# Optimization experiments

Hardware: AMD Instinct MI355X
Metric: run time of the kernel (lower is better)

The kernel has to match this reference:

```python
import jax, jax.numpy as jnp
import numpy as np
from jax import lax

EPS = 1e-5
HEADS = 8

def chan_ln(x, g):
    # ChanLayerNorm: normalize over channel dim (1), biased variance, gamma only
    mean = jnp.mean(x, axis=1, keepdims=True)
    var = jnp.var(x, axis=1, keepdims=True)
    return (x - mean) * lax.rsqrt(var + EPS) * g[None, :, None, None]

def conv1x1(x, w):  # w: [O, C]
    return jnp.einsum('bchw,oc->bohw', x, w)

def dwconv3(x, w):  # depthwise 3x3, w: [C,1,3,3]
    return lax.conv_general_dilated(x, w, (1, 1), 'SAME',
                                    dimension_numbers=('NCHW', 'OIHW', 'NCHW'),
                                    feature_group_count=x.shape[1])


def setup_inputs() -> dict:
    key = jax.random.key(0)
    ks = jax.random.split(key, 8)
    B, DIM, H, W = 8, 512, 96, 96
    INNER = 256
    s = 0.02
    return {
        'fmap': jax.random.normal(ks[0], (B, DIM, H, W), jnp.float32),
        'norm_g': jnp.ones((DIM,), jnp.float32),
        'q_w1': jax.random.normal(ks[1], (INNER, DIM), jnp.float32) * s,
        'q_wd': jax.random.normal(ks[2], (INNER, 1, 3, 3), jnp.float32) * s,
        'k_w1': jax.random.normal(ks[3], (INNER, DIM), jnp.float32) * s,
        'k_wd': jax.random.normal(ks[4], (INNER, 1, 3, 3), jnp.float32) * s,
        'v_w1': jax.random.normal(ks[5], (INNER, DIM), jnp.float32) * s,
        'v_wd': jax.random.normal(ks[6], (INNER, 1, 3, 3), jnp.float32) * s,
        'out_w': jax.random.normal(ks[7], (DIM, INNER), jnp.float32) * s,
        'out_norm_g': jnp.ones((DIM,), jnp.float32),
    }


def reference(fmap, norm_g, q_w1, q_wd, k_w1, k_wd, v_w1, v_wd, out_w, out_norm_g):
    B, C, H, W = fmap.shape
    inner = q_w1.shape[0]
    dh = inner // HEADS
    scale = dh ** -0.5

    x = chan_ln(fmap, norm_g)
    # dropout is identity in eval mode
    q = dwconv3(conv1x1(x, q_w1), q_wd)
    k = dwconv3(conv1x1(x, k_w1), k_wd)
    v = dwconv3(conv1x1(x, v_w1), v_wd)

    def split(t):  # [B, h*c, H, W] -> [B*h, N, c]
        return t.reshape(B, HEADS, dh, H * W).transpose(0, 1, 3, 2).reshape(B * HEADS, H * W, dh)

    q, k, v = split(q), split(k), split(v)
    q = jax.nn.softmax(q, axis=-1) * scale   # softmax over feature dim
    k = jax.nn.softmax(k, axis=-2)           # softmax over spatial dim

    context = jnp.einsum('bnd,bne->bde', k, v)   # [B*h, d, d]
    out = jnp.einsum('bnd,bde->bne', q, context) # [B*h, N, d]

    out = out.reshape(B, HEADS, H * W, dh).transpose(0, 1, 3, 2).reshape(B, inner, H, W)
    out = jax.nn.silu(out)
    out = conv1x1(out, out_w)
    return chan_ln(out, out_norm_g)
```

## Files before the change

### kernel.cpp

```cpp
#include <hip/hip_runtime.h>
#include <math.h>

#define BATCH 8
#define GB 4
#define CDIM 512
#define HGT 96
#define WID 96
#define HWN (HGT*WID)
#define INNER 256
#define NHEADS 8
#define DH 32
#define NPIX (BATCH*HWN)
#define EPSLN 1e-5f
#define QSCALE 0.17677669529663687f
#define PATHSZ ((size_t)GB*INNER*HWN)

typedef __bf16 bf16_t;
typedef bf16_t bf16x8 __attribute__((ext_vector_type(8)));
typedef float  f32x4  __attribute__((ext_vector_type(4)));

__device__ __forceinline__ void load_lds16(const bf16_t* gp, bf16_t* lp) {
    __builtin_amdgcn_global_load_lds(
        (const __attribute__((address_space(1))) unsigned int*)gp,
        (__attribute__((address_space(3))) unsigned int*)lp,
        16, 0, 0);
}

__global__ __launch_bounds__(256) void wsum_kernel(const float* __restrict__ qw,
                                                   const float* __restrict__ kw,
                                                   const float* __restrict__ vw,
                                                   const float* __restrict__ g,
                                                   float* __restrict__ wsum) {
    int i = blockIdx.x * 256 + threadIdx.x;
    if (i >= 3 * INNER) return;
    const float* w = (i < INNER) ? qw : (i < 2 * INNER) ? kw : vw;
    int o = i % INNER;
    float s = 0.f;
    for (int c = 0; c < CDIM; ++c) s += w[o * CDIM + c] * g[c];
    wsum[i] = s;
}

__global__ __launch_bounds__(256) void wprep_kernel(const float* __restrict__ qw,
                                                    const float* __restrict__ kw,
                                                    const float* __restrict__ vw,
                                                    const float* __restrict__ g,
                                                    const float* __restrict__ ow,
                                                    bf16_t* __restrict__ WB,
                                                    bf16_t* __restrict__ OWB) {
    int i = blockIdx.x * 256 + threadIdx.x;
    const int PS = INNER * CDIM;
    if (i < 3 * PS) {
        int m = i / PS;
        int idx = i % PS;
        int c = idx % CDIM;
        const float* w = (m == 0) ? qw : (m == 1) ? kw : vw;
        float val = w[idx] * g[c];
        bf16_t h = (bf16_t)val;
        bf16_t l = (bf16_t)(val - (float)h);
        WB[(size_t)(2 * m) * PS + idx] = h;
        WB[(size_t)(2 * m + 1) * PS + idx] = l;
    } else {
        int idx = i - 3 * PS;
        float val = ow[idx];
        bf16_t h = (bf16_t)val;
        bf16_t l = (bf16_t)(val - (float)h);
        OWB[idx] = h;
        OWB[PS + idx] = l;
    }
}

__global__ __launch_bounds__(256) void transpose_split_kernel(const float* __restrict__ X,
                                                              bf16_t* __restrict__ Fh,
                                                              bf16_t* __restrict__ Fl,
                                                              float* __restrict__ S1,
                                                              float* __restrict__ S2,
                                                              int pbase) {
    __shared__ float T[64][65];
    __shared__ float Ps[4][64], Ps2[4][64];
    int bb = blockIdx.z;
    int n0 = blockIdx.x * 64;
    int c0 = blockIdx.y * 64;
    const float* Xb = X + ((size_t)bb * CDIM) * HWN;
    int tid = threadIdx.x;
    int tx = tid & 63, ty = tid >> 6;
    #pragma unroll
    for (int cc = 0; cc < 64; cc += 4)
        T[cc + ty][tx] = Xb[(size_t)(c0 + cc + ty) * HWN + n0 + tx];
    __syncthreads();
    {
        float s = 0.f, s2 = 0.f;
        #pragma unroll
        for (int c = ty * 16; c < ty * 16 + 16; ++c) {
            float v = T[c][tx];
            s += v; s2 += v * v;
        }
        Ps[ty][tx] = s; Ps2[ty][tx] = s2;
    }
    __syncthreads();
    if (tid < 64) {
        float a = Ps[0][tid] + Ps[1][tid] + Ps[2][tid] + Ps[3][tid];
        float b = Ps2[0][tid] + Ps2[1][tid] + Ps2[2][tid] + Ps2[3][tid];
        int p = pbase + bb * HWN + n0 + tid;
        atomicAdd(&S1[p], a);
        atomicAdd(&S2[p], b);
    }
    int nr = tid >> 3;
    int c8 = (tid & 7) << 3;
    size_t obase = ((size_t)bb * HWN) * CDIM;
    #pragma unroll
    for (int half = 0; half < 2; ++half) {
        int n = nr + 32 * half;
        bf16x8 hv, lv;
        #pragma unroll
        for (int j = 0; j < 8; ++j) {
            float v = T[c8 + j][n];
            bf16_t h = (bf16_t)v;
            hv[j] = h;
            lv[j] = (bf16_t)(v - (float)h);
        }
        size_t off = obase + (size_t)(n0 + n) * CDIM + c0 + c8;
        *(bf16x8*)&Fh[off] = hv;
        *(bf16x8*)&Fl[off] = lv;
    }
}

template <int KDIM, int MROWS, int MODE>
__global__ __launch_bounds__(256) void mfma_gemm_kernel(const bf16_t* __restrict__ Wbase,
                                                        const bf16_t* __restrict__ Bh,
                                                        const bf16_t* __restrict__ Bl,
                                                        float* __restrict__ S1,
                                                        float* __restrict__ S2,
                                                        const float* __restrict__ wsum,
                                                        int pbase,
                                                        float* __restrict__ Ybase) {
    __shared__ bf16_t sA[2][128 * 32];
    __shared__ bf16_t sB[2][128 * 32];
    int bb = blockIdx.z;
    int n0 = blockIdx.x * 128;
    const int PS = INNER * CDIM;
    int o0, path;
    const bf16_t *Ah, *Al;
    float* Y;
    if (MODE == 0) {
        path = blockIdx.y >> 1;
        o0 = (blockIdx.y & 1) * 128;
        Ah = Wbase + (size_t)(2 * path) * PS;
        Al = Wbase + (size_t)(2 * path + 1) * PS;
        Y = Ybase + (size_t)path * PATHSZ;
        wsum += path * INNER;
    } else {
        path = 0;
        o0 = blockIdx.y * 128;
        Ah = Wbase;
        Al = Wbase + PS;
        Y = Ybase;
    }
    int tid = threadIdx.x;
    int wv = tid >> 6, ln = tid & 63;
    int wm = wv >> 1, wn = wv & 1;
    int quad = ln >> 4, lm = ln & 15;
    int srow = ln >> 2;
    int scol = (ln & 3) * 8;

    const bf16_t* Bhb = Bh + ((size_t)bb * HWN) * KDIM;
    const bf16_t* Blb = Bl + ((size_t)bb * HWN) * KDIM;

    f32x4 acc[4][4] = {};

    for (int c0 = 0; c0 < KDIM; c0 += 32) {
        __syncthreads();
        #pragma unroll
        for (int t = 0; t < 2; ++t) {
            int inst = wv * 2 + t;
            int row = inst * 16 + srow;
            size_t goA = (size_t)(o0 + row) * KDIM + c0 + scol;
            size_t goB = (size_t)(n0 + row) * KDIM + c0 + scol;
            load_lds16(&Ah[goA],  &sA[0][inst * 512]);
            load_lds16(&Al[goA],  &sA[1][inst * 512]);
            load_lds16(&Bhb[goB], &sB[0][inst * 512]);
            load_lds16(&Blb[goB], &sB[1][inst * 512]);
        }
        __syncthreads();

        bf16x8 afh[4], afl[4], bfh[4], bfl[4];
        #pragma unroll
        for (int i = 0; i < 4; ++i) {
            int o_l = wm * 64 + i * 16 + lm;
            afh[i] = *(const bf16x8*)&sA[0][o_l * 32 + quad * 8];
            afl[i] = *(const bf16x8*)&sA[1][o_l * 32 + quad * 8];
            int n_l = wn * 64 + i * 16 + lm;
            bfh[i] = *(const bf16x8*)&sB[0][n_l * 32 + quad * 8];
            bfl[i] = *(const bf16x8*)&sB[1][n_l * 32 + quad * 8];
        }
        #pragma unroll
        for (int i = 0; i < 4; ++i)
            #pragma unroll
            for (int j = 0; j < 4; ++j) {
                acc[i][j] = __builtin_amdgcn_mfma_f32_16x16x32_bf16(afh[i], bfh[j], acc[i][j], 0, 0, 0);
                acc[i][j] = __builtin_amdgcn_mfma_f32_16x16x32_bf16(afh[i], bfl[j], acc[i][j], 0, 0, 0);
                acc[i][j] = __builtin_amdgcn_mfma_f32_16x16x32_bf16(afl[i], bfh[j], acc[i][j], 0, 0, 0);
            }
    }

    float* Yb = Y + ((size_t)bb * MROWS) * HWN;
    __shared__ float Sn[128], Sn2[128];
    if (MODE == 1) {
        if (tid < 128) Sn[tid] = 0.f; else Sn2[tid - 128] = 0.f;
        __syncthreads();
    }
    #pragma unroll
    for (int j = 0; j < 4; ++j) {
        int nl = wn * 64 + j * 16 + lm;
        int n = n0 + nl;
        float mn = 0.f, rs = 0.f;
        if (MODE == 0) {
            int p = pbase + bb * HWN + n;
            float s1 = S1[p], s2 = S2[p];
            mn = s1 * (1.0f / CDIM);
            float var = s2 * (1.0f / CDIM) - mn * mn;
            rs = rsqrtf(var + EPSLN);
        }
        float js = 0.f, js2 = 0.f;
        #pragma unroll
        for (int i = 0; i < 4; ++i) {
            #pragma unroll
            for (int r = 0; r < 4; ++r) {
                int o = o0 + wm * 64 + i * 16 + quad * 4 + r;
                float v = acc[i][j][r];
                if (MODE == 0) v = rs * (v - mn * wsum[o]);
                Yb[(size_t)o * HWN + n] = v;
                if (MODE == 1) { js += v; js2 += v * v; }
            }
        }
        if (MODE == 1) {
            atomicAdd(&Sn[nl], js);
            atomicAdd(&Sn2[nl], js2);
        }
    }
    if (MODE == 1) {
        __syncthreads();
        if (tid < 128) {
            int p = pbase + bb * HWN + n0 + tid;
            atomicAdd(&S1[p], Sn[tid]);
            atomicAdd(&S2[p], Sn2[tid]);
        }
    }
}

__global__ __launch_bounds__(256) void dwconv_kernel(const float* __restrict__ A3,
                                                     const float* __restrict__ qwd,
                                                     const float* __restrict__ kwd,
                                                     const float* __restrict__ vwd,
                                                     float* __restrict__ D3,
                                                     float* __restrict__ Ssum,
                                                     int bo) {
    int c = blockIdx.y;
    int zz = blockIdx.z;
    int path = zz >> 2;
    int bb = zz & 3;
    const float* wf = ((path == 0) ? qwd : (path == 1) ? kwd : vwd) + c * 9;
    float w[9];
    #pragma unroll
    for (int j = 0; j < 9; ++j) w[j] = wf[j];

    int n0 = (blockIdx.x << 10) + (threadIdx.x << 2);
    int y = n0 / WID;
    int x0 = n0 - y * WID;
    bool hasL = (x0 != 0);
    bool hasR = (x0 != WID - 4);

    const float* bp = A3 + (size_t)path * PATHSZ + (size_t)(bb * INNER + c) * HWN;
    float o0 = 0.f, o1 = 0.f, o2 = 0.f, o3 = 0.f;
    #pragma unroll
    for (int dy = 0; dy < 3; ++dy) {
        int yy = y + dy - 1;
        if ((unsigned)yy < HGT) {
            const float* r = bp + yy * WID + x0;
            f32x4 cv = *(const f32x4*)r;
            float lft = hasL ? r[-1] : 0.f;
            float rgt = hasR ? r[4]  : 0.f;
            float w0 = w[3 * dy], w1 = w[3 * dy + 1], w2 = w[3 * dy + 2];
            o0 += lft  * w0 + cv.x * w1 + cv.y * w2;
            o1 += cv.x * w0 + cv.y * w1 + cv.z * w2;
            o2 += cv.y * w0 + cv.z * w1 + cv.w * w2;
            o3 += cv.z * w0 + cv.w * w1 + rgt  * w2;
        }
    }

    size_t oi = (size_t)path * PATHSZ + (size_t)(bb * INNER + c) * HWN + n0;
    if (path == 1) {
        float e0 = __expf(o0), e1 = __expf(o1), e2 = __expf(o2), e3 = __expf(o3);
        *(f32x4*)&D3[oi] = (f32x4){e0, e1, e2, e3};
        float s = e0 + e1 + e2 + e3;
        #pragma unroll
        for (int off2 = 32; off2; off2 >>= 1) s += __shfl_down(s, off2);
        __shared__ float red[4];
        int lane = threadIdx.x & 63, wvi = threadIdx.x >> 6;
        if (lane == 0) red[wvi] = s;
        __syncthreads();
        if (threadIdx.x == 0)
            atomicAdd(&Ssum[(bo + bb) * INNER + c], red[0] + red[1] + red[2] + red[3]);
    } else {
        *(f32x4*)&D3[oi] = (f32x4){o0, o1, o2, o3};
    }
}

__global__ __launch_bounds__(256) void context_kernel(const float* __restrict__ K,
                                                      const float* __restrict__ V,
                                                      float* __restrict__ ctxp) {
    int seg = blockIdx.x;
    int bh = blockIdx.y;
    int bb = bh / NHEADS, h = bh % NHEADS;
    const float* kb = K + ((size_t)bb * INNER + h * DH) * HWN;
    const float* vb = V + ((size_t)bb * INNER + h * DH) * HWN;
    __shared__ float kt[DH][64];
    __shared__ float vt[DH][65];
    int tid = threadIdx.x;
    int e = tid & 31;
    int d0 = tid >> 5;
    float acc[4] = {0.f, 0.f, 0.f, 0.f};
    for (int ch = 0; ch < 9; ++ch) {
        int n0 = seg * 576 + ch * 64;
        __syncthreads();
        #pragma unroll
        for (int j = 0; j < 8; ++j) {
            int idx = tid + 256 * j;
            int d = idx >> 6, nn = idx & 63;
            kt[d][nn] = kb[(size_t)d * HWN + n0 + nn];
            vt[d][nn] = vb[(size_t)d * HWN + n0 + nn];
        }
        __syncthreads();
        for (int nn = 0; nn < 64; ++nn) {
            float vv = vt[e][nn];
            #pragma unroll
            for (int i = 0; i < 4; ++i) acc[i] += kt[d0 + 8 * i][nn] * vv;
        }
    }
    #pragma unroll
    for (int i = 0; i < 4; ++i)
        ctxp[(((size_t)bh * 16 + seg) * DH + d0 + 8 * i) * DH + e] = acc[i];
}

__global__ __launch_bounds__(256) void ctxreduce_kernel(const float* __restrict__ ctxp,
                                                        const float* __restrict__ Ssum,
                                                        int bo,
                                                        float* __restrict__ ctx) {
    int i = blockIdx.x * 256 + threadIdx.x;
    int bh = i >> 10, de = i & 1023;
    int d = de >> 5;
    int bb = bh / NHEADS, h = bh % NHEADS;
    float s = 0.f;
    #pragma unroll
    for (int seg = 0; seg < 16; ++seg) s += ctxp[((size_t)bh * 16 + seg) * 1024 + de];
    float S = Ssum[(bo + bb) * INNER + h * DH + d];
    ctx[i] = s / S;
}

__global__ __launch_bounds__(256) void qctx_kernel(const float* __restrict__ Q,
                                                   const float* __restrict__ ctx,
                                                   bf16_t* __restrict__ Oh,
                                                   bf16_t* __restrict__ Ol) {
    int bh = blockIdx.y;
    int bb = bh / NHEADS, h = bh % NHEADS;
    int n = blockIdx.x * 256 + threadIdx.x;
    __shared__ float cs[DH * DH];
    for (int j = threadIdx.x; j < DH * DH; j += 256) cs[j] = ctx[(size_t)bh * DH * DH + j];
    __syncthreads();
    const float* qb = Q + ((size_t)bb * INNER + h * DH) * HWN + n;
    float qv[DH];
    float mx = -1e30f;
    #pragma unroll
    for (int d = 0; d < DH; ++d) { qv[d] = qb[(size_t)d * HWN]; mx = fmaxf(mx, qv[d]); }
    float s = 0.f;
    #pragma unroll
    for (int d = 0; d < DH; ++d) { qv[d] = __expf(qv[d] - mx); s += qv[d]; }
    float inv = QSCALE / s;
    float acc[DH];
    #pragma unroll
    for (int e = 0; e < DH; ++e) acc[e] = 0.f;
    #pragma unroll
    for (int d = 0; d < DH; ++d) {
        float q = qv[d] * inv;
        #pragma unroll
        for (int e = 0; e < DH; ++e) acc[e] += q * cs[d * DH + e];
    }
    size_t ob = ((size_t)bb * HWN + n) * INNER + h * DH;
    bf16x8 hv, lv;
    #pragma unroll
    for (int e8 = 0; e8 < 4; ++e8) {
        #pragma unroll
        for (int e = 0; e < 8; ++e) {
            float x = acc[e8 * 8 + e];
            float sl = x / (1.0f + __expf(-x));
            bf16_t h = (bf16_t)sl;
            hv[e] = h;
            lv[e] = (bf16_t)(sl - (float)h);
        }
        *(bf16x8*)&Oh[ob + e8 * 8] = hv;
        *(bf16x8*)&Ol[ob + e8 * 8] = lv;
    }
}

__global__ __launch_bounds__(256) void norm_kernel(const float* __restrict__ X,
                                                   const float* __restrict__ S1,
                                                   const float* __restrict__ S2,
                                                   const float* __restrict__ g,
                                                   float* __restrict__ out,
                                                   int pbase) {
    size_t i = ((size_t)blockIdx.x * 256 + threadIdx.x) * 4;
    int n = (int)(i % HWN);
    size_t bc = i / HWN;
    int c = (int)(bc % CDIM);
    int bb = (int)(bc / CDIM);
    int p = pbase + bb * HWN + n;
    f32x4 x  = *(const f32x4*)&X[i];
    f32x4 s1 = *(const f32x4*)&S1[p];
    f32x4 s2 = *(const f32x4*)&S2[p];
    float gc = g[c];
    f32x4 o;
    #pragma unroll
    for (int j = 0; j < 4; ++j) {
        float m = s1[j] * (1.0f / CDIM);
        float var = s2[j] * (1.0f / CDIM) - m * m;
        float rs = rsqrtf(var + EPSLN);
        o[j] = (x[j] - m) * rs * gc;
    }
    *(f32x4*)&out[i] = o;
}

extern "C" void kernel_launch(void* const* d_in, const int* in_sizes, int n_in,
                              void* d_out, int out_size, void* d_ws, size_t ws_size,
                              hipStream_t stream) {
    const float* fmap       = (const float*)d_in[0];
    const float* norm_g     = (const float*)d_in[1];
    const float* q_w1       = (const float*)d_in[2];
    const float* q_wd       = (const float*)d_in[3];
    const float* k_w1       = (const float*)d_in[4];
    const float* k_wd       = (const float*)d_in[5];
    const float* v_w1       = (const float*)d_in[6];
    const float* v_wd       = (const float*)d_in[7];
    const float* out_w      = (const float*)d_in[8];
    const float* out_norm_g = (const float*)d_in[9];
    float* out = (float*)d_out;

    float* ws = (float*)d_ws;
    size_t off = 0;
    auto alloc = [&](size_t n) { float* p = ws + off; off += n; return p; };
    float* S1   = alloc(73728);
    float* S2   = alloc(73728);
    float* S1o  = alloc(73728);
    float* S2o  = alloc(73728);
    float* Ssum = alloc(2048);
    const size_t ZERON = 73728ull * 4 + 2048;
    float* wsum = alloc(768);
    bf16_t* WB  = (bf16_t*)alloc(393216);
    bf16_t* OWB = (bf16_t*)alloc(131072);
    float* ctxp = alloc(524288);
    float* ctx  = alloc(32768);
    bf16_t* Fh  = (bf16_t*)alloc(9437184);
    bf16_t* Fl  = (bf16_t*)alloc(9437184);
    float* A3   = alloc(3 * 9437184);
    float* D3   = alloc(3 * 9437184);
    bf16_t* Oh  = (bf16_t*)alloc(4718592);
    bf16_t* Ol  = (bf16_t*)alloc(4718592);
    float* CONV2 = alloc(18874368);

    dim3 blk(256);
    hipMemsetAsync(S1, 0, ZERON * sizeof(float), stream);
    wsum_kernel<<<dim3(3), blk, 0, stream>>>(q_w1, k_w1, v_w1, norm_g, wsum);
    wprep_kernel<<<dim3(2048), blk, 0, stream>>>(q_w1, k_w1, v_w1, norm_g, out_w, WB, OWB);

    for (int g = 0; g < 2; ++g) {
        const float* fmg = fmap + (size_t)g * GB * CDIM * HWN;
        int pbase = g * GB * HWN;
        int bo = g * GB;

        transpose_split_kernel<<<dim3(144, 8, GB), blk, 0, stream>>>(fmg, Fh, Fl, S1, S2, pbase);

        mfma_gemm_kernel<CDIM, INNER, 0><<<dim3(72, 6, GB), blk, 0, stream>>>(
            WB, Fh, Fl, S1, S2, wsum, pbase, A3);

        dwconv_kernel<<<dim3(HWN / 1024, INNER, 3 * GB), blk, 0, stream>>>(
            A3, q_wd, k_wd, v_wd, D3, Ssum, bo);

        context_kernel<<<dim3(16, GB * NHEADS), blk, 0, stream>>>(
            D3 + PATHSZ, D3 + 2 * PATHSZ, ctxp);
        ctxreduce_kernel<<<dim3(GB * NHEADS * 1024 / 256), blk, 0, stream>>>(
            ctxp, Ssum, bo, ctx);
        qctx_kernel<<<dim3(HWN / 256, GB * NHEADS), blk, 0, stream>>>(D3, ctx, Oh, Ol);

        mfma_gemm_kernel<INNER, CDIM, 1><<<dim3(72, 4, GB), blk, 0, stream>>>(
            OWB, Oh, Ol, S1o, S2o, nullptr, pbase, CONV2);

        norm_kernel<<<dim3(GB * CDIM * HWN / 1024), blk, 0, stream>>>(
            CONV2, S1o, S2o, out_norm_g, out + (size_t)g * GB * CDIM * HWN, pbase);
    }
}
```

Baseline: 871.2 us.

## Vectorize transpose loads, swizzle GEMM LDS, and compute two rows per dwconv thread

The transpose kernel now reads the input with 16-byte vector loads instead of scalar loads. The MFMA GEMM applies an XOR swizzle to the LDS column offsets on both the global-to-LDS store and the fragment reads, to cut LDS bank conflicts. The depthwise conv is relaunched with 24x8 thread blocks, and each thread computes two output rows from four loaded input rows, so the overlapping row loads are shared. The tradeoffs are more registers per dwconv thread, a smaller block that gives a different reduction layout for the K softmax sum, and a swizzle that must match exactly between the write and read sides.

```diff
diff --git a/kernel.cpp b/kernel.cpp
--- a/kernel.cpp
+++ b/kernel.cpp
@@ -82,10 +82,20 @@
     int c0 = blockIdx.y * 64;
     const float* Xb = X + ((size_t)bb * CDIM) * HWN;
     int tid = threadIdx.x;
+    {
+        int nl4 = (tid & 15) * 4;
+        int cl = tid >> 4;
+        #pragma unroll
+        for (int it = 0; it < 4; ++it) {
+            int cc = cl + 16 * it;
+            f32x4 v = *(const f32x4*)&Xb[(size_t)(c0 + cc) * HWN + n0 + nl4];
+            T[cc][nl4]     = v.x;
+            T[cc][nl4 + 1] = v.y;
+            T[cc][nl4 + 2] = v.z;
+            T[cc][nl4 + 3] = v.w;
+        }
+    }
     int tx = tid & 63, ty = tid >> 6;
-    #pragma unroll
-    for (int cc = 0; cc < 64; cc += 4)
-        T[cc + ty][tx] = Xb[(size_t)(c0 + cc + ty) * HWN + n0 + tx];
     __syncthreads();
     {
         float s = 0.f, s2 = 0.f;
@@ -160,7 +170,8 @@
     int wm = wv >> 1, wn = wv & 1;
     int quad = ln >> 4, lm = ln & 15;
     int srow = ln >> 2;
-    int scol = (ln & 3) * 8;
+    int scol = ((ln & 3) ^ ((ln >> 3) & 3)) * 8;
+    int qs = (quad ^ ((lm >> 1) & 3)) * 8;
 
     const bf16_t* Bhb = Bh + ((size_t)bb * HWN) * KDIM;
     const bf16_t* Blb = Bl + ((size_t)bb * HWN) * KDIM;
@@ -186,11 +197,11 @@
         #pragma unroll
         for (int i = 0; i < 4; ++i) {
             int o_l = wm * 64 + i * 16 + lm;
-            afh[i] = *(const bf16x8*)&sA[0][o_l * 32 + quad * 8];
-            afl[i] = *(const bf16x8*)&sA[1][o_l * 32 + quad * 8];
+            afh[i] = *(const bf16x8*)&sA[0][o_l * 32 + qs];
+            afl[i] = *(const bf16x8*)&sA[1][o_l * 32 + qs];
             int n_l = wn * 64 + i * 16 + lm;
-            bfh[i] = *(const bf16x8*)&sB[0][n_l * 32 + quad * 8];
-            bfl[i] = *(const bf16x8*)&sB[1][n_l * 32 + quad * 8];
+            bfh[i] = *(const bf16x8*)&sB[0][n_l * 32 + qs];
+            bfl[i] = *(const bf16x8*)&sB[1][n_l * 32 + qs];
         }
         #pragma unroll
         for (int i = 0; i < 4; ++i)
@@ -247,7 +258,7 @@
     }
 }
 
-__global__ __launch_bounds__(256) void dwconv_kernel(const float* __restrict__ A3,
+__global__ __launch_bounds__(192) void dwconv_kernel(const float* __restrict__ A3,
                                                      const float* __restrict__ qwd,
                                                      const float* __restrict__ kwd,
                                                      const float* __restrict__ vwd,
@@ -263,45 +274,70 @@
     #pragma unroll
     for (int j = 0; j < 9; ++j) w[j] = wf[j];
 
-    int n0 = (blockIdx.x << 10) + (threadIdx.x << 2);
-    int y = n0 / WID;
-    int x0 = n0 - y * WID;
+    int x0 = threadIdx.x * 4;
+    int y0 = (blockIdx.x * 8 + threadIdx.y) * 2;
     bool hasL = (x0 != 0);
     bool hasR = (x0 != WID - 4);
 
     const float* bp = A3 + (size_t)path * PATHSZ + (size_t)(bb * INNER + c) * HWN;
-    float o0 = 0.f, o1 = 0.f, o2 = 0.f, o3 = 0.f;
-    #pragma unroll
-    for (int dy = 0; dy < 3; ++dy) {
-        int yy = y + dy - 1;
+    f32x4 r[4];
+    float L[4], R[4];
+    #pragma unroll
+    for (int dy = 0; dy < 4; ++dy) {
+        int yy = y0 + dy - 1;
         if ((unsigned)yy < HGT) {
-            const float* r = bp + yy * WID + x0;
-            f32x4 cv = *(const f32x4*)r;
-            float lft = hasL ? r[-1] : 0.f;
-            float rgt = hasR ? r[4]  : 0.f;
+            const float* rp = bp + yy * WID + x0;
+            r[dy] = *(const f32x4*)rp;
+            L[dy] = hasL ? rp[-1] : 0.f;
+            R[dy] = hasR ? rp[4]  : 0.f;
+        } else {
+            r[dy] = (f32x4){0.f, 0.f, 0.f, 0.f};
+            L[dy] = 0.f; R[dy] = 0.f;
+        }
+    }
+
+    f32x4 o[2];
+    #pragma unroll
+    for (int orow = 0; orow < 2; ++orow) {
+        float a0 = 0.f, a1 = 0.f, a2 = 0.f, a3 = 0.f;
+        #pragma unroll
+        for (int dy = 0; dy < 3; ++dy) {
+            f32x4 cv = r[orow + dy];
+            float lf = L[orow + dy], rg = R[orow + dy];
             float w0 = w[3 * dy], w1 = w[3 * dy + 1], w2 = w[3 * dy + 2];
-            o0 += lft  * w0 + cv.x * w1 + cv.y * w2;
-            o1 += cv.x * w0 + cv.y * w1 + cv.z * w2;
-            o2 += cv.y * w0 + cv.z * w1 + cv.w * w2;
-            o3 += cv.z * w0 + cv.w * w1 + rgt  * w2;
-        }
-    }
-
-    size_t oi = (size_t)path * PATHSZ + (size_t)(bb * INNER + c) * HWN + n0;
+            a0 += lf   * w0 + cv.x * w1 + cv.y * w2;
+            a1 += cv.x * w0 + cv.y * w1 + cv.z * w2;
+            a2 += cv.y * w0 + cv.z * w1 + cv.w * w2;
+            a3 += cv.z * w0 + cv.w * w1 + rg   * w2;
+        }
+        o[orow] = (f32x4){a0, a1, a2, a3};
+    }
+
+    size_t ob = (size_t)path * PATHSZ + (size_t)(bb * INNER + c) * HWN;
     if (path == 1) {
-        float e0 = __expf(o0), e1 = __expf(o1), e2 = __expf(o2), e3 = __expf(o3);
-        *(f32x4*)&D3[oi] = (f32x4){e0, e1, e2, e3};
-        float s = e0 + e1 + e2 + e3;
+        float s = 0.f;
+        #pragma unroll
+        for (int orow = 0; orow < 2; ++orow) {
+            #pragma unroll
+            for (int j = 0; j < 4; ++j) {
+                float e = __expf(o[orow][j]);
+                o[orow][j] = e;
+                s += e;
+            }
+            *(f32x4*)&D3[ob + (size_t)(y0 + orow) * WID + x0] = o[orow];
+        }
         #pragma unroll
         for (int off2 = 32; off2; off2 >>= 1) s += __shfl_down(s, off2);
-        __shared__ float red[4];
-        int lane = threadIdx.x & 63, wvi = threadIdx.x >> 6;
+        __shared__ float red[3];
+        int tid = threadIdx.y * 24 + threadIdx.x;
+        int lane = tid & 63, wvi = tid >> 6;
         if (lane == 0) red[wvi] = s;
         __syncthreads();
-        if (threadIdx.x == 0)
-            atomicAdd(&Ssum[(bo + bb) * INNER + c], red[0] + red[1] + red[2] + red[3]);
+        if (tid == 0)
+            atomicAdd(&Ssum[(bo + bb) * INNER + c], red[0] + red[1] + red[2]);
     } else {
-        *(f32x4*)&D3[oi] = (f32x4){o0, o1, o2, o3};
+        *(f32x4*)&D3[ob + (size_t)y0 * WID + x0] = o[0];
+        *(f32x4*)&D3[ob + (size_t)(y0 + 1) * WID + x0] = o[1];
     }
 }
 
@@ -480,7 +516,7 @@
         mfma_gemm_kernel<CDIM, INNER, 0><<<dim3(72, 6, GB), blk, 0, stream>>>(
             WB, Fh, Fl, S1, S2, wsum, pbase, A3);
 
-        dwconv_kernel<<<dim3(HWN / 1024, INNER, 3 * GB), blk, 0, stream>>>(
+        dwconv_kernel<<<dim3(HGT / 16, INNER, 3 * GB), dim3(24, 8), 0, stream>>>(
             A3, q_wd, k_wd, v_wd, D3, Ssum, bo);
 
         context_kernel<<<dim3(16, GB * NHEADS), blk, 0, stream>>>(
```

After: 878.9 us. Within noise of the previous version (+0.9%).
